# Kernel optimization log

Measured on AMD Instinct MI355X. Metric: run time of the kernel, lower is better.

The kernel has to match this reference:

```python
import jax, jax.numpy as jnp
import numpy as np

NOISE_DIM = 128
IN_FEATURES = 512
OUT_FEATURES = 512
BATCH = 256


def setup_inputs() -> dict:
    key = jax.random.key(0)
    k1, k2, k3 = jax.random.split(key, 3)
    out_dim = IN_FEATURES * OUT_FEATURES + OUT_FEATURES
    # x = [noise | features]
    x = jax.random.normal(k1, (BATCH, NOISE_DIM + IN_FEATURES), dtype=jnp.float32)
    # hypermodel Linear params; scale ~ 1/sqrt(fan_in) like torch default init
    scale = 1.0 / np.sqrt(NOISE_DIM)
    W = jax.random.uniform(k2, (NOISE_DIM, out_dim), dtype=jnp.float32, minval=-scale, maxval=scale)
    b = jax.random.uniform(k3, (out_dim,), dtype=jnp.float32, minval=-scale, maxval=scale)
    return {"x": x, "W": W, "b": b}


def reference(x, W, b):
    # split input into hypernet noise and features
    noise = x[:, :NOISE_DIM]            # [B, noise_dim]
    feats = x[:, NOISE_DIM:]            # [B, in_features]
    # hypermodel: generate per-sample linear params
    params = noise @ W + b              # [B, in*out + out]
    w_flat = params[:, : IN_FEATURES * OUT_FEATURES]
    bias = params[:, IN_FEATURES * OUT_FEATURES :]        # [B, out]
    weight = w_flat.reshape(-1, IN_FEATURES, OUT_FEATURES)  # [B, in, out]
    # batched matmul (torch.bmm of [B,1,in] @ [B,in,out]) + bias, squeeze
    out = jnp.einsum("bi,bio->bo", feats, weight) + bias   # [B, out]
    return out
```

## Files before the change

### kernel.cpp

```cpp
#include <hip/hip_runtime.h>
#include <hip/hip_bf16.h>
#include <stdint.h>

namespace {
constexpr int kBatch = 256;
constexpr int kNoise = 128;
constexpr int kIn    = 512;
constexpr int kOut   = 512;
constexpr int kXCols = kNoise + kIn;
constexpr int kPCols = kIn * kOut + kOut;
constexpr int kOTile = 32;
constexpr int kITile = 16;
constexpr int kSplits = kIn / kITile;
constexpr int kWStride = 68;
constexpr int kFeatsStride = 260;
}

typedef __bf16 bf16x8 __attribute__((ext_vector_type(8)));
typedef float  f32x2  __attribute__((ext_vector_type(2)));
typedef float  f32x4  __attribute__((ext_vector_type(4)));
typedef unsigned int u32x4 __attribute__((ext_vector_type(4)));

__device__ inline unsigned int pack_bf16x2(float lo, float hi) {
    unsigned int a = (unsigned int)__builtin_bit_cast(unsigned short, (__bf16)lo);
    unsigned int b = (unsigned int)__builtin_bit_cast(unsigned short, (__bf16)hi);
    return a | (b << 16);
}

__device__ inline void wg_barrier_lds() {
    __asm__ volatile("" ::: "memory");
    __builtin_amdgcn_s_waitcnt(0xC07F);
    __builtin_amdgcn_s_barrier();
    __asm__ volatile("" ::: "memory");
}

__global__ __launch_bounds__(1024, 8)
void hyper_gemm_kernel(const float* __restrict__ x,
                       const float* __restrict__ W,
                       const float* __restrict__ bvec,
                       float* __restrict__ part)
{
    const int tid  = threadIdx.x;
    const int lane = tid & 63;
    const int wave = tid >> 6;
    const int q    = lane >> 4;
    const int l16  = lane & 15;

    const int o0 = blockIdx.x * kOTile;
    const int i0 = blockIdx.y * kITile;

    const int u  = tid >> 4;
    const int c2 = (tid & 15) * 2;

    __shared__ unsigned int wtile[2][kOTile * kWStride];
    __shared__ float feats_lds[kITile * kFeatsStride];
    __shared__ float bv_lds[(kITile + 1) * kOTile];

    const int nPass = (blockIdx.y == 0) ? (kITile + 1) : kITile;

    auto pass_cbase = [&](int p) -> size_t {
        return (p == kITile) ? (size_t)(kIn * kOut) : (size_t)(i0 + p) * kOut;
    };
    auto wrow = [&](int p) -> const float* {
        return W + (size_t)(2 * u) * kPCols + pass_cbase(p) + o0 + c2;
    };

    f32x2 pa0, pa1, pb0, pb1;
    { const float* wp = wrow(0); pa0 = *(const f32x2*)wp; pa1 = *(const f32x2*)(wp + kPCols); }
    { const float* wp = wrow(1); pb0 = *(const f32x2*)wp; pb1 = *(const f32x2*)(wp + kPCols); }

    for (int idx = tid; idx < (kITile + 1) * kOTile; idx += 1024) {
        const int p = idx >> 5, c = idx & 31;
        const size_t cb = (p == kITile) ? (size_t)(kIn * kOut) : (size_t)(i0 + p) * kOut;
        bv_lds[idx] = bvec[cb + o0 + c];
    }

    {
        const int i    = tid & 15;
        const int brow = tid >> 4;
        #pragma unroll
        for (int rep = 0; rep < 4; ++rep) {
            const int b = brow + rep * 64;
            feats_lds[i * kFeatsStride + b] = x[b * kXCols + kNoise + i0 + i];
        }
    }

    bf16x8 afrag[4];
    {
        const float* xr = x + (size_t)(wave * 16 + l16) * kXCols;
        #pragma unroll
        for (int s = 0; s < 4; ++s) {
            const float* p = xr + s * 32 + q * 8;
            f32x4 u0 = *(const f32x4*)(p);
            f32x4 u1 = *(const f32x4*)(p + 4);
            bf16x8 a;
            a[0] = (__bf16)u0[0]; a[1] = (__bf16)u0[1];
            a[2] = (__bf16)u0[2]; a[3] = (__bf16)u0[3];
            a[4] = (__bf16)u1[0]; a[5] = (__bf16)u1[1];
            a[6] = (__bf16)u1[2]; a[7] = (__bf16)u1[3];
            afrag[s] = a;
        }
    }

    float oacc[2][4];
    #pragma unroll
    for (int nt = 0; nt < 2; ++nt)
        #pragma unroll
        for (int r = 0; r < 4; ++r) oacc[nt][r] = 0.f;

    __syncthreads();

    for (int ip = 0; ip < nPass; ++ip) {
        unsigned int pk0 = pack_bf16x2(pa0[0], pa1[0]);
        unsigned int pk1 = pack_bf16x2(pa0[1], pa1[1]);

        unsigned int* wt = &wtile[ip & 1][0];
        wt[(c2    ) * kWStride + u] = pk0;
        wt[(c2 + 1) * kWStride + u] = pk1;

        pa0 = pb0; pa1 = pb1;
        if (ip + 2 < nPass) {
            const float* wp = wrow(ip + 2);
            pb0 = *(const f32x2*)wp; pb1 = *(const f32x2*)(wp + kPCols);
        }

        wg_barrier_lds();

        f32x4 acc[2];
        const f32x4 zero = {0.f, 0.f, 0.f, 0.f};
        acc[0] = zero; acc[1] = zero;

        #pragma unroll
        for (int s = 0; s < 4; ++s) {
            #pragma unroll
            for (int nt = 0; nt < 2; ++nt) {
                u32x4 raw = *(const u32x4*)&wt[(nt * 16 + l16) * kWStride + s * 16 + q * 4];
                bf16x8 bfrag = __builtin_bit_cast(bf16x8, raw);
                acc[nt] = __builtin_amdgcn_mfma_f32_16x16x32_bf16(
                    afrag[s], bfrag, acc[nt], 0, 0, 0);
            }
        }

        const float bv0 = bv_lds[ip * kOTile + l16];
        const float bv1 = bv_lds[ip * kOTile + 16 + l16];

        if (ip < kITile) {
            const f32x4 f4 = *(const f32x4*)&feats_lds[ip * kFeatsStride
                                    + wave * 16 + q * 4];
            #pragma unroll
            for (int r = 0; r < 4; ++r) {
                oacc[0][r] += f4[r] * (acc[0][r] + bv0);
                oacc[1][r] += f4[r] * (acc[1][r] + bv1);
            }
        } else {
            #pragma unroll
            for (int r = 0; r < 4; ++r) {
                oacc[0][r] += acc[0][r] + bv0;
                oacc[1][r] += acc[1][r] + bv1;
            }
        }
    }

    float* pp = part + (size_t)blockIdx.y * kBatch * kOut;
    #pragma unroll
    for (int nt = 0; nt < 2; ++nt) {
        const int o = o0 + nt * 16 + l16;
        #pragma unroll
        for (int r = 0; r < 4; ++r) {
            const int b = wave * 16 + q * 4 + r;
            pp[(size_t)b * kOut + o] = oacc[nt][r];
        }
    }
}

__global__ __launch_bounds__(256)
void reduce_kernel(const float* __restrict__ part, float* __restrict__ out)
{
    const size_t idx4 = ((size_t)blockIdx.x * 256 + threadIdx.x) * 4;
    f32x4 acc = *(const f32x4*)(part + idx4);
    #pragma unroll
    for (int s = 1; s < kSplits; ++s)
        acc += *(const f32x4*)(part + (size_t)s * kBatch * kOut + idx4);
    *(f32x4*)(out + idx4) = acc;
}

extern "C" void kernel_launch(void* const* d_in, const int* in_sizes, int n_in,
                              void* d_out, int out_size, void* d_ws, size_t ws_size,
                              hipStream_t stream) {
    const float* x  = (const float*)d_in[0];
    const float* W  = (const float*)d_in[1];
    const float* bv = (const float*)d_in[2];
    float* out  = (float*)d_out;
    float* part = (float*)d_ws;

    dim3 grid(kOut / kOTile, kSplits);
    hyper_gemm_kernel<<<grid, 1024, 0, stream>>>(x, W, bv, part);

    const int n4 = kBatch * kOut / 4;
    reduce_kernel<<<n4 / 256, 256, 0, stream>>>(part, out);
}
```

Baseline: 216.6 us.

## Halve GEMM block threads, give each wave two row tiles, deepen W prefetch

The hypernet GEMM block shrinks from 1024 to 512 threads, and each wave now covers two 16-row batch tiles that share each B fragment read from LDS. W staging now uses float4 loads with a three-stage register prefetch instead of two. Partial slabs are padded by 64 floats to avoid bank or channel aliasing, and the reduce kernel uses 128-thread blocks. The aim is better LDS fragment reuse and memory-level parallelism in exchange for more registers per thread and fewer waves per block.

```diff
diff --git a/kernel.cpp b/kernel.cpp
--- a/kernel.cpp
+++ b/kernel.cpp
@@ -14,10 +14,10 @@
 constexpr int kSplits = kIn / kITile;
 constexpr int kWStride = 68;
 constexpr int kFeatsStride = 260;
+constexpr int kSlab = kBatch * kOut + 64;
 }
 
 typedef __bf16 bf16x8 __attribute__((ext_vector_type(8)));
-typedef float  f32x2  __attribute__((ext_vector_type(2)));
 typedef float  f32x4  __attribute__((ext_vector_type(4)));
 typedef unsigned int u32x4 __attribute__((ext_vector_type(4)));
 
@@ -34,7 +34,7 @@
     __asm__ volatile("" ::: "memory");
 }
 
-__global__ __launch_bounds__(1024, 8)
+__global__ __launch_bounds__(512, 4)
 void hyper_gemm_kernel(const float* __restrict__ x,
                        const float* __restrict__ W,
                        const float* __restrict__ bvec,
@@ -49,8 +49,8 @@
     const int o0 = blockIdx.x * kOTile;
     const int i0 = blockIdx.y * kITile;
 
-    const int u  = tid >> 4;
-    const int c2 = (tid & 15) * 2;
+    const int u  = tid >> 3;
+    const int c4 = (tid & 7) * 4;
 
     __shared__ unsigned int wtile[2][kOTile * kWStride];
     __shared__ float feats_lds[kITile * kFeatsStride];
@@ -62,14 +62,15 @@
         return (p == kITile) ? (size_t)(kIn * kOut) : (size_t)(i0 + p) * kOut;
     };
     auto wrow = [&](int p) -> const float* {
-        return W + (size_t)(2 * u) * kPCols + pass_cbase(p) + o0 + c2;
+        return W + (size_t)(2 * u) * kPCols + pass_cbase(p) + o0 + c4;
     };
 
-    f32x2 pa0, pa1, pb0, pb1;
-    { const float* wp = wrow(0); pa0 = *(const f32x2*)wp; pa1 = *(const f32x2*)(wp + kPCols); }
-    { const float* wp = wrow(1); pb0 = *(const f32x2*)wp; pb1 = *(const f32x2*)(wp + kPCols); }
-
-    for (int idx = tid; idx < (kITile + 1) * kOTile; idx += 1024) {
+    f32x4 pA0, pA1, pB0, pB1, pC0, pC1;
+    { const float* wp = wrow(0); pA0 = *(const f32x4*)wp; pA1 = *(const f32x4*)(wp + kPCols); }
+    { const float* wp = wrow(1); pB0 = *(const f32x4*)wp; pB1 = *(const f32x4*)(wp + kPCols); }
+    { const float* wp = wrow(2); pC0 = *(const f32x4*)wp; pC1 = *(const f32x4*)(wp + kPCols); }
+
+    for (int idx = tid; idx < (kITile + 1) * kOTile; idx += 512) {
         const int p = idx >> 5, c = idx & 31;
         const size_t cb = (p == kITile) ? (size_t)(kIn * kOut) : (size_t)(i0 + p) * kOut;
         bv_lds[idx] = bvec[cb + o0 + c];
@@ -79,15 +80,16 @@
         const int i    = tid & 15;
         const int brow = tid >> 4;
         #pragma unroll
-        for (int rep = 0; rep < 4; ++rep) {
-            const int b = brow + rep * 64;
+        for (int rep = 0; rep < 8; ++rep) {
+            const int b = brow + rep * 32;
             feats_lds[i * kFeatsStride + b] = x[b * kXCols + kNoise + i0 + i];
         }
     }
 
-    bf16x8 afrag[4];
-    {
-        const float* xr = x + (size_t)(wave * 16 + l16) * kXCols;
+    bf16x8 afrag[2][4];
+    #pragma unroll
+    for (int rt = 0; rt < 2; ++rt) {
+        const float* xr = x + (size_t)(wave * 32 + rt * 16 + l16) * kXCols;
         #pragma unroll
         for (int s = 0; s < 4; ++s) {
             const float* p = xr + s * 32 + q * 8;
@@ -98,37 +100,43 @@
             a[2] = (__bf16)u0[2]; a[3] = (__bf16)u0[3];
             a[4] = (__bf16)u1[0]; a[5] = (__bf16)u1[1];
             a[6] = (__bf16)u1[2]; a[7] = (__bf16)u1[3];
-            afrag[s] = a;
-        }
-    }
-
-    float oacc[2][4];
-    #pragma unroll
-    for (int nt = 0; nt < 2; ++nt)
-        #pragma unroll
-        for (int r = 0; r < 4; ++r) oacc[nt][r] = 0.f;
+            afrag[rt][s] = a;
+        }
+    }
+
+    float oacc[2][2][4];
+    #pragma unroll
+    for (int rt = 0; rt < 2; ++rt)
+        #pragma unroll
+        for (int nt = 0; nt < 2; ++nt)
+            #pragma unroll
+            for (int r = 0; r < 4; ++r) oacc[rt][nt][r] = 0.f;
 
     __syncthreads();
 
     for (int ip = 0; ip < nPass; ++ip) {
-        unsigned int pk0 = pack_bf16x2(pa0[0], pa1[0]);
-        unsigned int pk1 = pack_bf16x2(pa0[1], pa1[1]);
+        unsigned int pk0 = pack_bf16x2(pA0[0], pA1[0]);
+        unsigned int pk1 = pack_bf16x2(pA0[1], pA1[1]);
+        unsigned int pk2 = pack_bf16x2(pA0[2], pA1[2]);
+        unsigned int pk3 = pack_bf16x2(pA0[3], pA1[3]);
 
         unsigned int* wt = &wtile[ip & 1][0];
-        wt[(c2    ) * kWStride + u] = pk0;
-        wt[(c2 + 1) * kWStride + u] = pk1;
-
-        pa0 = pb0; pa1 = pb1;
-        if (ip + 2 < nPass) {
-            const float* wp = wrow(ip + 2);
-            pb0 = *(const f32x2*)wp; pb1 = *(const f32x2*)(wp + kPCols);
+        wt[(c4 + 0) * kWStride + u] = pk0;
+        wt[(c4 + 1) * kWStride + u] = pk1;
+        wt[(c4 + 2) * kWStride + u] = pk2;
+        wt[(c4 + 3) * kWStride + u] = pk3;
+
+        pA0 = pB0; pA1 = pB1; pB0 = pC0; pB1 = pC1;
+        if (ip + 3 < nPass) {
+            const float* wp = wrow(ip + 3);
+            pC0 = *(const f32x4*)wp; pC1 = *(const f32x4*)(wp + kPCols);
         }
 
         wg_barrier_lds();
 
-        f32x4 acc[2];
+        f32x4 acc[2][2];
         const f32x4 zero = {0.f, 0.f, 0.f, 0.f};
-        acc[0] = zero; acc[1] = zero;
+        acc[0][0] = zero; acc[0][1] = zero; acc[1][0] = zero; acc[1][1] = zero;
 
         #pragma unroll
         for (int s = 0; s < 4; ++s) {
@@ -136,8 +144,10 @@
             for (int nt = 0; nt < 2; ++nt) {
                 u32x4 raw = *(const u32x4*)&wt[(nt * 16 + l16) * kWStride + s * 16 + q * 4];
                 bf16x8 bfrag = __builtin_bit_cast(bf16x8, raw);
-                acc[nt] = __builtin_amdgcn_mfma_f32_16x16x32_bf16(
-                    afrag[s], bfrag, acc[nt], 0, 0, 0);
+                acc[0][nt] = __builtin_amdgcn_mfma_f32_16x16x32_bf16(
+                    afrag[0][s], bfrag, acc[0][nt], 0, 0, 0);
+                acc[1][nt] = __builtin_amdgcn_mfma_f32_16x16x32_bf16(
+                    afrag[1][s], bfrag, acc[1][nt], 0, 0, 0);
             }
         }
 
@@ -145,42 +155,49 @@
         const float bv1 = bv_lds[ip * kOTile + 16 + l16];
 
         if (ip < kITile) {
-            const f32x4 f4 = *(const f32x4*)&feats_lds[ip * kFeatsStride
-                                    + wave * 16 + q * 4];
-            #pragma unroll
-            for (int r = 0; r < 4; ++r) {
-                oacc[0][r] += f4[r] * (acc[0][r] + bv0);
-                oacc[1][r] += f4[r] * (acc[1][r] + bv1);
+            #pragma unroll
+            for (int rt = 0; rt < 2; ++rt) {
+                const f32x4 f4 = *(const f32x4*)&feats_lds[ip * kFeatsStride
+                                        + wave * 32 + rt * 16 + q * 4];
+                #pragma unroll
+                for (int r = 0; r < 4; ++r) {
+                    oacc[rt][0][r] += f4[r] * (acc[rt][0][r] + bv0);
+                    oacc[rt][1][r] += f4[r] * (acc[rt][1][r] + bv1);
+                }
             }
         } else {
             #pragma unroll
+            for (int rt = 0; rt < 2; ++rt)
+                #pragma unroll
+                for (int r = 0; r < 4; ++r) {
+                    oacc[rt][0][r] += acc[rt][0][r] + bv0;
+                    oacc[rt][1][r] += acc[rt][1][r] + bv1;
+                }
+        }
+    }
+
+    float* pp = part + (size_t)blockIdx.y * kSlab;
+    #pragma unroll
+    for (int rt = 0; rt < 2; ++rt)
+        #pragma unroll
+        for (int nt = 0; nt < 2; ++nt) {
+            const int o = o0 + nt * 16 + l16;
+            #pragma unroll
             for (int r = 0; r < 4; ++r) {
-                oacc[0][r] += acc[0][r] + bv0;
-                oacc[1][r] += acc[1][r] + bv1;
+                const int b = wave * 32 + rt * 16 + q * 4 + r;
+                pp[(size_t)b * kOut + o] = oacc[rt][nt][r];
             }
         }
-    }
-
-    float* pp = part + (size_t)blockIdx.y * kBatch * kOut;
-    #pragma unroll
-    for (int nt = 0; nt < 2; ++nt) {
-        const int o = o0 + nt * 16 + l16;
-        #pragma unroll
-        for (int r = 0; r < 4; ++r) {
-            const int b = wave * 16 + q * 4 + r;
-            pp[(size_t)b * kOut + o] = oacc[nt][r];
-        }
-    }
-}
-
-__global__ __launch_bounds__(256)
+}
+
+__global__ __launch_bounds__(128)
 void reduce_kernel(const float* __restrict__ part, float* __restrict__ out)
 {
-    const size_t idx4 = ((size_t)blockIdx.x * 256 + threadIdx.x) * 4;
+    const size_t idx4 = ((size_t)blockIdx.x * 128 + threadIdx.x) * 4;
     f32x4 acc = *(const f32x4*)(part + idx4);
     #pragma unroll
     for (int s = 1; s < kSplits; ++s)
-        acc += *(const f32x4*)(part + (size_t)s * kBatch * kOut + idx4);
+        acc += *(const f32x4*)(part + (size_t)s * kSlab + idx4);
     *(f32x4*)(out + idx4) = acc;
 }
 
@@ -194,8 +211,8 @@
     float* part = (float*)d_ws;
 
     dim3 grid(kOut / kOTile, kSplits);
-    hyper_gemm_kernel<<<grid, 1024, 0, stream>>>(x, W, bv, part);
+    hyper_gemm_kernel<<<grid, 512, 0, stream>>>(x, W, bv, part);
 
     const int n4 = kBatch * kOut / 4;
-    reduce_kernel<<<n4 / 256, 256, 0, stream>>>(part, out);
-}
+    reduce_kernel<<<n4 / 128, 128, 0, stream>>>(part, out);
+}
```

After: 213.0 us. About the same (-1.7%).
